# Kernel tuning notes

Hardware: AMD Instinct MI355X
Metric: run time of the kernel (lower is better)

## Reference

```python
import jax, jax.numpy as jnp
import numpy as np

B, T, STEPS = 4096, 56, 28
H, ANN, ENC, DEC = 126, 30, 20, 15
DIN = 1 + DEC + H  # decoder GRU input width = 142


def _gru_step(h, x, Wih, Whh, bih, bhh):
    # torch GRU cell math; Wih: [3H, in], Whh: [3H, H]
    gi = x @ Wih.T + bih
    gh = h @ Whh.T + bhh
    ir, iz, inn = jnp.split(gi, 3, axis=-1)
    hr, hz, hn = jnp.split(gh, 3, axis=-1)
    r = jax.nn.sigmoid(ir + hr)
    z = jax.nn.sigmoid(iz + hz)
    n = jnp.tanh(inn + r * hn)
    return (1.0 - z) * n + z * h


def setup_inputs() -> dict:
    key = jax.random.key(0)
    ks = jax.random.split(key, 23)
    p = lambda k, s: jax.random.normal(k, s, dtype=jnp.float32) * 0.08
    return {
        "ann_data": jax.random.normal(ks[0], (B, ANN), dtype=jnp.float32),
        "encoder_data": jax.random.normal(ks[1], (T, B, ENC), dtype=jnp.float32),
        "decoder_data": jax.random.normal(ks[2], (STEPS, B, DEC), dtype=jnp.float32),
        "s2h_W1": p(ks[3], (96, ANN)), "s2h_b1": p(ks[4], (96,)),
        "s2h_W2": p(ks[5], (H, 96)), "s2h_b2": p(ks[6], (H,)),
        "enc_Wih": p(ks[7], (3 * H, ENC)), "enc_Whh": p(ks[8], (3 * H, H)),
        "enc_bih": p(ks[9], (3 * H,)), "enc_bhh": p(ks[10], (3 * H,)),
        "dec_Wih": p(ks[11], (3 * H, DIN)), "dec_Whh": p(ks[12], (3 * H, H)),
        "dec_bih": p(ks[13], (3 * H,)), "dec_bhh": p(ks[14], (3 * H,)),
        "U_W": p(ks[15], (H, H)), "U_b": p(ks[16], (H,)),
        "Wl_W": p(ks[17], (H, H)), "Wl_b": p(ks[18], (H,)),
        "V_W": p(ks[19], (1, H)), "V_b": p(ks[20], (1,)),
        "h2o_W": p(ks[21], (1, H)), "h2o_b": p(ks[22], (1,)),
    }


def reference(ann_data, encoder_data, decoder_data,
              s2h_W1, s2h_b1, s2h_W2, s2h_b2,
              enc_Wih, enc_Whh, enc_bih, enc_bhh,
              dec_Wih, dec_Whh, dec_bih, dec_bhh,
              U_W, U_b, Wl_W, Wl_b, V_W, V_b, h2o_W, h2o_b):
    # static -> initial hidden: Linear(ANN,96) -> ReLU -> Linear(96,H)
    hidden = jnp.maximum(ann_data @ s2h_W1.T + s2h_b1, 0.0) @ s2h_W2.T + s2h_b2  # [B,H]

    def enc_f(h, x):
        h2 = _gru_step(h, x, enc_Wih, enc_Whh, enc_bih, enc_bhh)
        return h2, h2

    hidden, enc_out = jax.lax.scan(enc_f, hidden, encoder_data)  # enc_out: [T,B,H]

    Uo = enc_out @ U_W.T + U_b            # [T,B,H] precomputed (loop-invariant)
    gt0 = encoder_data[-1, :, 0:1]        # initial_ground, [B,1]

    def dec_f(carry, dec_x):
        h, prev = carry
        Wh = h @ Wl_W.T + Wl_b                              # [B,H]
        scores = jnp.tanh(Uo + Wh[None]) @ V_W.T + V_b      # [T,B,1]
        alpha = jax.nn.softmax(scores, axis=0)              # softmax over time
        attn = jnp.einsum('tb,tbh->bh', alpha[..., 0], enc_out)
        x = jnp.concatenate([prev, dec_x, attn], axis=1)    # [B,DIN]
        h2 = _gru_step(h, x, dec_Wih, dec_Whh, dec_bih, dec_bhh)
        out = h2 @ h2o_W.T + h2o_b                          # [B,1]
        return (h2, out), out

    _, outputs = jax.lax.scan(dec_f, (hidden, gt0), decoder_data)
    return outputs  # [STEPS, B, 1]
```

## Files before the change

### kernel.cpp

```cpp
#include <hip/hip_runtime.h>
#include <stdint.h>

typedef unsigned int u32;
typedef unsigned short u16;
typedef _Float16 f16;
typedef _Float16 f16x8 __attribute__((ext_vector_type(8)));
typedef _Float16 f16x4 __attribute__((ext_vector_type(4)));
typedef _Float16 f16x2 __attribute__((ext_vector_type(2)));
typedef float f32x4 __attribute__((ext_vector_type(4)));

constexpr int NB = 4096;
constexpr int NT = 56;
constexpr int NS = 28;
constexpr int NH = 126;
constexpr int NHP = 128;
constexpr float LOG2E = 1.4426950408889634f;

constexpr int LROW = 136;
constexpr int LB   = NT * LROW + 8;

constexpr size_t OFF_H    = 0;
constexpr size_t OFF_ENC  = 2097152;
constexpr size_t OFF_UO   = OFF_ENC + 58720256;
constexpr size_t OFF_WENC = OFF_UO + 58720256;
constexpr size_t OFF_WDEC = OFF_WENC + 122880;
constexpr size_t OFF_WL   = OFF_WDEC + 221184;
constexpr size_t OFF_UW   = OFF_WL + 32768;

__device__ __forceinline__ float fexp2(float x){ return __builtin_amdgcn_exp2f(x); }
__device__ __forceinline__ float frcp (float x){ return __builtin_amdgcn_rcpf(x); }
__device__ __forceinline__ float sigm (float x){ return frcp(1.f + fexp2(-LOG2E * x)); }
__device__ __forceinline__ float ftanh(float x){ return 1.f - 2.f * frcp(1.f + fexp2(2.f * LOG2E * x)); }
__device__ __forceinline__ float asf(u32 u){ union { u32 i; float f; } v; v.i = u; return v.f; }
__device__ __forceinline__ u16 tobf(float f){ union { float f; u32 i; } v; v.f = f;
  return (u16)((v.i + 0x7fffu + ((v.i >> 16) & 1u)) >> 16); }

__global__ void k_prep(const float* __restrict__ eWih, const float* __restrict__ eWhh,
                       const float* __restrict__ dWih, const float* __restrict__ dWhh,
                       const float* __restrict__ UW,   const float* __restrict__ Wl,
                       char* __restrict__ ws)
{
  f16* wenc = (f16*)(ws + OFF_WENC);
  f16* wdec = (f16*)(ws + OFF_WDEC);
  f16* wl   = (f16*)(ws + OFF_WL);
  f16* uw   = (f16*)(ws + OFF_UW);
  const int nE = 384 * 160, nD = 384 * 288, nW = 128 * 128;
  const int total = nE + nD + nW + nW;
  for (int i = blockIdx.x * 256 + threadIdx.x; i < total; i += gridDim.x * 256) {
    int idx = i;
    if (idx < nE) {
      const int r = idx / 160, c = idx % 160;
      float v = 0.f;
      if (r < 378) {
        if (c < 20) v = eWih[r * 20 + c];
        else if (c >= 32 && c < 158) v = eWhh[r * 126 + (c - 32)];
      }
      wenc[idx] = (f16)v; continue;
    }
    idx -= nE;
    if (idx < nD) {
      const int r = idx / 288, c = idx % 288;
      float v = 0.f;
      if (r < 378) {
        if (c < 16) v = dWih[r * 142 + c];
        else if (c >= 32 && c < 158) v = dWih[r * 142 + 16 + (c - 32)];
        else if (c >= 160 && c < 286) v = dWhh[r * 126 + (c - 160)];
      }
      wdec[idx] = (f16)v; continue;
    }
    idx -= nD;
    if (idx < nW) {
      const int r = idx >> 7, c = idx & 127;
      wl[idx] = (f16)((r < 126 && c < 126) ? Wl[r * 126 + c] : 0.f);
      continue;
    }
    idx -= nW;
    { const int r = idx >> 7, c = idx & 127;
      uw[idx] = (f16)((r < 126 && c < 126) ? UW[r * 126 + c] : 0.f); }
  }
}

__global__ __launch_bounds__(256) void k_mlp(
    const float* __restrict__ ann, const float* __restrict__ W1, const float* __restrict__ b1,
    const float* __restrict__ W2, const float* __restrict__ b2, float* __restrict__ hstate)
{
  __shared__ float anns[32][33];
  __shared__ float t1s[32][101];
  const int tid = threadIdx.x;
  const int b0 = blockIdx.x * 32;
  for (int i = tid; i < 32 * 30; i += 256)
    anns[i / 30][i % 30] = ann[(b0 + i / 30) * 30 + (i % 30)];
  __syncthreads();
  const int b = tid & 31, rg = tid >> 5;
  for (int m = rg; m < 96; m += 8) {
    float a = b1[m];
    for (int k = 0; k < 30; ++k) a += W1[m * 30 + k] * anns[b][k];
    t1s[b][m] = fmaxf(a, 0.f);
  }
  __syncthreads();
  for (int j = rg; j < NHP; j += 8) {
    float a = 0.f;
    if (j < NH) {
      a = b2[j];
      for (int k = 0; k < 96; ++k) a += W2[j * 96 + k] * t1s[b][k];
    }
    hstate[(b0 + b) * NHP + j] = a;
  }
}

__global__ __launch_bounds__(512) void k_enc(
    const float* __restrict__ xenc, const f16* __restrict__ Wenc,
    const f16* __restrict__ Uw,
    const float* __restrict__ bih, const float* __restrict__ bhh,
    const float* __restrict__ Ub,
    float* __restrict__ hstate, f16* __restrict__ encO, u16* __restrict__ uoO)
{
  __shared__ f16 av[16][296];
  const int tid = threadIdx.x;
  const int wid = tid >> 6, l = tid & 63, quad = l >> 4, col = l & 15;
  const int b0 = blockIdx.x * 16;
  const int jb = wid * 16, j = jb + col;
  const bool valid = j < NH;
  const int jc = valid ? j : NH - 1;

  const float br  = bih[jc]        + bhh[jc];
  const float bz  = bih[NH + jc]   + bhh[NH + jc];
  const float bnx = bih[2*NH + jc];
  const float bnh = bhh[2*NH + jc];
  const float ub  = Ub[jc];

  f16x8 rB[5], zB[5], nxB, nhB[4], uB[4];
  {
    const int ko = quad * 8, rr = jb + col;
#pragma unroll
    for (int kt = 0; kt < 5; ++kt) {
      rB[kt] = *(const f16x8*)&Wenc[rr * 160 + kt * 32 + ko];
      zB[kt] = *(const f16x8*)&Wenc[(NH + rr) * 160 + kt * 32 + ko];
    }
    nxB = *(const f16x8*)&Wenc[(2*NH + rr) * 160 + ko];
#pragma unroll
    for (int kt = 0; kt < 4; ++kt) {
      nhB[kt] = *(const f16x8*)&Wenc[(2*NH + rr) * 160 + 32 + kt * 32 + ko];
      uB[kt]  = *(const f16x8*)&Uw[rr * 128 + kt * 32 + ko];
    }
  }

  {
    const int bb = tid >> 5, c4 = (tid & 31) * 4;
    const float4 hv = *(const float4*)&hstate[(b0 + bb) * NHP + c4];
    av[bb][32 + c4]     = (f16)hv.x; av[bb][32 + c4 + 1] = (f16)hv.y;
    av[bb][32 + c4 + 2] = (f16)hv.z; av[bb][32 + c4 + 3] = (f16)hv.w;
  }
  if (tid < 192) { const int bb = tid / 12, p = tid % 12; av[bb][20 + p] = (f16)0.f; }
  __syncthreads();

  const int m = col, ko = quad * 8;
  for (int t = 0; t < NT; ++t) {
    const int hp = 32 + (t & 1) * 128, hq = 32 + ((t + 1) & 1) * 128;
    if (tid < 320) {
      const int bb = tid / 20, e = tid % 20;
      av[bb][e] = (f16)xenc[((size_t)t * NB + b0 + bb) * 20 + e];
    }
    __syncthreads();
    f16x8 A[5];
    A[0] = *(const f16x8*)&av[m][ko];
#pragma unroll
    for (int kt = 1; kt < 5; ++kt) A[kt] = *(const f16x8*)&av[m][hp + (kt - 1) * 32 + ko];

    f32x4 Cr = {br, br, br, br}, Cz = {bz, bz, bz, bz};
    f32x4 Cnx = {bnx, bnx, bnx, bnx}, Cnh = {bnh, bnh, bnh, bnh};
#pragma unroll
    for (int kt = 0; kt < 5; ++kt) {
      Cr = __builtin_amdgcn_mfma_f32_16x16x32_f16(A[kt], rB[kt], Cr, 0, 0, 0);
      Cz = __builtin_amdgcn_mfma_f32_16x16x32_f16(A[kt], zB[kt], Cz, 0, 0, 0);
    }
    Cnx = __builtin_amdgcn_mfma_f32_16x16x32_f16(A[0], nxB, Cnx, 0, 0, 0);
#pragma unroll
    for (int kt = 0; kt < 4; ++kt)
      Cnh = __builtin_amdgcn_mfma_f32_16x16x32_f16(A[kt + 1], nhB[kt], Cnh, 0, 0, 0);

    float hv4[4];
#pragma unroll
    for (int c = 0; c < 4; ++c) {
      const int bb = quad * 4 + c;
      const float hold = (float)av[bb][hp + j];
      const float r = sigm(Cr[c]), z = sigm(Cz[c]);
      const float n = ftanh(Cnx[c] + r * Cnh[c]);
      hv4[c] = (1.f - z) * n + z * hold;
    }
#pragma unroll
    for (int c = 0; c < 4; ++c) {
      const int bb = quad * 4 + c;
      const f16 hs = valid ? (f16)hv4[c] : (f16)0.f;
      av[bb][hq + j] = hs;
      encO[((size_t)(b0 + bb) * NT + t) * 128 + j] = hs;
    }
    if (t == NT - 1 && valid) {
#pragma unroll
      for (int c = 0; c < 4; ++c)
        hstate[(b0 + quad * 4 + c) * NHP + j] = hv4[c];
    }
    __syncthreads();

    f16x8 Ah[4];
#pragma unroll
    for (int kt = 0; kt < 4; ++kt) Ah[kt] = *(const f16x8*)&av[m][hq + kt * 32 + ko];
    f32x4 Cu = {ub, ub, ub, ub};
#pragma unroll
    for (int kt = 0; kt < 4; ++kt)
      Cu = __builtin_amdgcn_mfma_f32_16x16x32_f16(Ah[kt], uB[kt], Cu, 0, 0, 0);
#pragma unroll
    for (int c = 0; c < 4; ++c) {
      const u16 eu = tobf(fexp2(2.f * LOG2E * Cu[c]));
      uoO[((size_t)(b0 + quad * 4 + c) * NT + t) * 128 + j] = valid ? eu : (u16)0;
    }
  }
}

__global__ __launch_bounds__(512) void k_dec(
    const float* __restrict__ xdec, const float* __restrict__ xenc,
    const f16* __restrict__ Wdec, const f16* __restrict__ WlW,
    const float* __restrict__ bih, const float* __restrict__ bhh,
    const float* __restrict__ Wlb, const float* __restrict__ Vw,
    const float* __restrict__ Vb, const float* __restrict__ how,
    const float* __restrict__ hob, const float* __restrict__ hstate,
    const f16* __restrict__ encO, const u16* __restrict__ uoO,
    float* __restrict__ out)
{
  __shared__ __align__(16) u16 uoL[4 * LB];
  __shared__ __align__(16) f16 encL[4 * LB];
  __shared__ __align__(16) f16 av[5][424];
  __shared__ float EWS[4][132];
  __shared__ float scS[4][68];
  __shared__ __align__(16) f16 hows16[128];
  const int tid = threadIdx.x;
  const int wid = tid >> 6, l = tid & 63, quad = l >> 4, col = l & 15;
  const int b0 = blockIdx.x * 4;
  const int jb = wid * 16, j = jb + col;
  const bool valid = j < NH;
  const int jc = valid ? j : NH - 1;

  const float br  = bih[jc]        + bhh[jc];
  const float bz  = bih[NH + jc]   + bhh[NH + jc];
  const float bnx = bih[2*NH + jc];
  const float bnh = bhh[2*NH + jc];
  const float wb  = Wlb[jc];
  const float vb0 = Vb[0], hob0 = hob[0];

  f16x8 rB[9], zB[9], nxB[5], nhB[4], wlB[4];
  {
    const int ko = quad * 8, rr = jb + col;
#pragma unroll
    for (int kt = 0; kt < 9; ++kt) {
      rB[kt] = *(const f16x8*)&Wdec[rr * 288 + kt * 32 + ko];
      zB[kt] = *(const f16x8*)&Wdec[(NH + rr) * 288 + kt * 32 + ko];
    }
#pragma unroll
    for (int kt = 0; kt < 5; ++kt)
      nxB[kt] = *(const f16x8*)&Wdec[(2*NH + rr) * 288 + kt * 32 + ko];
#pragma unroll
    for (int kt = 0; kt < 4; ++kt) {
      nhB[kt] = *(const f16x8*)&Wdec[(2*NH + rr) * 288 + 160 + kt * 32 + ko];
      wlB[kt] = *(const f16x8*)&WlW[rr * 128 + kt * 32 + ko];
    }
  }

  const int g = tid >> 3, sub = tid & 7;
  float n2v[16], svsum = 0.f;
#pragma unroll
  for (int i = 0; i < 16; ++i) {
    const int jj = sub * 16 + i;
    const float v = (jj < NH) ? Vw[jj] : 0.f;
    n2v[i] = -2.f * v;
    svsum += v;
  }
  if (tid >= 256 && tid < 384) {
    const int q = tid - 256; hows16[q] = (f16)((q < NH) ? how[q] : 0.f);
  }
  for (int i = tid; i < 5 * 424; i += 512) av[i / 424][i % 424] = (f16)0.f;
  if (tid < 24) EWS[tid / 6][126 + tid % 6] = 0.f;
  {
    const size_t gb = (size_t)b0 * NT * 128;
    for (int i = tid; i < 4 * NT * 16; i += 512) {
      const int ch = i & 15, btr = i >> 4;
      const int bb = btr / NT, tt = btr % NT;
      const int dst = bb * LB + tt * LROW + ch * 8;
      const size_t src = gb + (size_t)btr * 128 + ch * 8;
      *(f16x8*)&uoL [dst] = *(const f16x8*)&uoO [src];
      *(f16x8*)&encL[dst] = *(const f16x8*)&encO[src];
    }
  }
  __syncthreads();
  if (tid < 128) {
    const int bb = tid >> 5, c4 = (tid & 31) * 4;
    const float4 hv = *(const float4*)&hstate[(b0 + bb) * NHP + c4];
    av[bb][160 + c4]     = (f16)hv.x; av[bb][160 + c4 + 1] = (f16)hv.y;
    av[bb][160 + c4 + 2] = (f16)hv.z; av[bb][160 + c4 + 3] = (f16)hv.w;
  }
  if (tid < 4) av[tid][0] = (f16)xenc[((size_t)(NT - 1) * NB + b0 + tid) * 20];
  __syncthreads();

  const int m = col, ko = quad * 8;
  const int arow = (m < 4) ? m : 4;
  const int pb = tid & 3, pth = (tid >> 2) & 1, pjp = tid >> 3;

  for (int s = 0; s < NS; ++s) {
    const int hp = 160 + (s & 1) * 128, hq = 160 + ((s + 1) & 1) * 128;

    {
      f16x8 Ah[4];
#pragma unroll
      for (int kt = 0; kt < 4; ++kt) Ah[kt] = *(const f16x8*)&av[arow][hp + kt * 32 + ko];
      f32x4 Cw = {wb, wb, wb, wb};
#pragma unroll
      for (int kt = 0; kt < 4; ++kt)
        Cw = __builtin_amdgcn_mfma_f32_16x16x32_f16(Ah[kt], wlB[kt], Cw, 0, 0, 0);
      if (quad == 0 && valid) {
#pragma unroll
        for (int c = 0; c < 4; ++c) EWS[c][j] = fexp2(2.f * LOG2E * Cw[c]);
      }
    }
    if (tid < 60) { const int bb = tid / 15, e = tid % 15;
      av[bb][1 + e] = (f16)xdec[((size_t)s * NB + b0 + bb) * 15 + e]; }
    __syncthreads();

    {
      const int sbb = g & 3, tb = g >> 2;
      float ew[16];
#pragma unroll
      for (int i = 0; i < 4; ++i)
        *(float4*)&ew[i * 4] = *(const float4*)&EWS[sbb][sub * 16 + i * 4];
      const u16* up0 = &uoL[sbb * LB + sub * 16];
#pragma unroll
      for (int rd = 0; rd < 4; ++rd) {
        const int t = rd * 16 + tb;
        if (t < NT) {
          const u16* up = up0 + t * LROW;
          const uint4 q0 = *(const uint4*)&up[0];
          const uint4 q1 = *(const uint4*)&up[8];
          float acc = svsum;
          const u32 wsv[8] = {q0.x, q0.y, q0.z, q0.w, q1.x, q1.y, q1.z, q1.w};
#pragma unroll
          for (int k = 0; k < 8; ++k) {
            const float p0 = fmaf(asf(wsv[k] << 16),         ew[2 * k],     1.f);
            const float p1 = fmaf(asf(wsv[k] & 0xffff0000u), ew[2 * k + 1], 1.f);
            acc = fmaf(n2v[2 * k],     frcp(p0), acc);
            acc = fmaf(n2v[2 * k + 1], frcp(p1), acc);
          }
          acc += __shfl_xor(acc, 1, 64);
          acc += __shfl_xor(acc, 2, 64);
          acc += __shfl_xor(acc, 4, 64);
          if (sub == 0) scS[sbb][t] = acc + vb0;
        }
      }
    }
    __syncthreads();

    {
      const int j0 = pjp * 2;
      const f16* er = &encL[pb * LB + j0];
      const float* scp = &scS[pb][pth * 28];
      const int tbase = pth * 28;
      float Z = 0.f, a0 = 0.f, a1 = 0.f;
#pragma unroll
      for (int i2 = 0; i2 < 28; i2 += 2) {
        const float2 scv = *(const float2*)&scp[i2];
        const float e0 = fexp2(LOG2E * scv.x);
        const float e1 = fexp2(LOG2E * scv.y);
        Z += e0 + e1;
        const f16x2 v0 = *(const f16x2*)&er[(tbase + i2    ) * LROW];
        const f16x2 v1 = *(const f16x2*)&er[(tbase + i2 + 1) * LROW];
        a0 += e0 * (float)v0[0] + e1 * (float)v1[0];
        a1 += e0 * (float)v0[1] + e1 * (float)v1[1];
      }
      a0 += __shfl_xor(a0, 4, 64);
      a1 += __shfl_xor(a1, 4, 64);
      Z  += __shfl_xor(Z, 4, 64);
      if (pth == 0) {
        const float inv = frcp(Z);
        f16x2 st; st[0] = (f16)(a0 * inv); st[1] = (f16)(a1 * inv);
        *(f16x2*)&av[pb][32 + j0] = st;
      }
    }
    __syncthreads();

    {
      f16x8 A[9];
#pragma unroll
      for (int kt = 0; kt < 5; ++kt) A[kt] = *(const f16x8*)&av[arow][kt * 32 + ko];
#pragma unroll
      for (int kt = 5; kt < 9; ++kt) A[kt] = *(const f16x8*)&av[arow][hp + (kt - 5) * 32 + ko];
      f32x4 Cr = {br, br, br, br}, Cz = {bz, bz, bz, bz};
      f32x4 Cnx = {bnx, bnx, bnx, bnx}, Cnh = {bnh, bnh, bnh, bnh};
#pragma unroll
      for (int kt = 0; kt < 9; ++kt) {
        Cr = __builtin_amdgcn_mfma_f32_16x16x32_f16(A[kt], rB[kt], Cr, 0, 0, 0);
        Cz = __builtin_amdgcn_mfma_f32_16x16x32_f16(A[kt], zB[kt], Cz, 0, 0, 0);
      }
#pragma unroll
      for (int kt = 0; kt < 5; ++kt)
        Cnx = __builtin_amdgcn_mfma_f32_16x16x32_f16(A[kt], nxB[kt], Cnx, 0, 0, 0);
#pragma unroll
      for (int kt = 0; kt < 4; ++kt)
        Cnh = __builtin_amdgcn_mfma_f32_16x16x32_f16(A[kt + 5], nhB[kt], Cnh, 0, 0, 0);
      if (quad == 0) {
#pragma unroll
        for (int c = 0; c < 4; ++c) {
          const float hold = (float)av[c][hp + j];
          const float r = sigm(Cr[c]), z = sigm(Cz[c]);
          const float n = ftanh(Cnx[c] + r * Cnh[c]);
          const float h2 = (1.f - z) * n + z * hold;
          if (valid) av[c][hq + j] = (f16)h2;
        }
      }
    }
    __syncthreads();

    if (wid == 0) {
      f16x8 Ah2[4], hB[4];
      const f16x8 zz = {};
#pragma unroll
      for (int kt = 0; kt < 4; ++kt) {
        Ah2[kt] = *(const f16x8*)&av[arow][hq + kt * 32 + ko];
        hB[kt] = (col == 0) ? *(const f16x8*)&hows16[kt * 32 + ko] : zz;
      }
      f32x4 Co = {0.f, 0.f, 0.f, 0.f};
#pragma unroll
      for (int kt = 0; kt < 4; ++kt)
        Co = __builtin_amdgcn_mfma_f32_16x16x32_f16(Ah2[kt], hB[kt], Co, 0, 0, 0);
      if (l == 0) {
#pragma unroll
        for (int c = 0; c < 4; ++c) {
          const float o = Co[c] + hob0;
          out[(size_t)s * NB + b0 + c] = o;
          av[c][0] = (f16)o;
        }
      }
    }
  }
}

extern "C" void kernel_launch(void* const* d_in, const int* in_sizes, int n_in,
                              void* d_out, int out_size, void* d_ws, size_t ws_size,
                              hipStream_t stream)
{
  const float* ann   = (const float*)d_in[0];
  const float* xenc  = (const float*)d_in[1];
  const float* xdec  = (const float*)d_in[2];
  const float* W1    = (const float*)d_in[3];
  const float* b1    = (const float*)d_in[4];
  const float* W2    = (const float*)d_in[5];
  const float* b2    = (const float*)d_in[6];
  const float* eWih  = (const float*)d_in[7];
  const float* eWhh  = (const float*)d_in[8];
  const float* ebih  = (const float*)d_in[9];
  const float* ebhh  = (const float*)d_in[10];
  const float* dWih  = (const float*)d_in[11];
  const float* dWhh  = (const float*)d_in[12];
  const float* dbih  = (const float*)d_in[13];
  const float* dbhh  = (const float*)d_in[14];
  const float* UW    = (const float*)d_in[15];
  const float* Ubias = (const float*)d_in[16];
  const float* Wl    = (const float*)d_in[17];
  const float* Wlb   = (const float*)d_in[18];
  const float* Vw    = (const float*)d_in[19];
  const float* Vb    = (const float*)d_in[20];
  const float* how   = (const float*)d_in[21];
  const float* hob   = (const float*)d_in[22];

  char* ws = (char*)d_ws;
  float* hstate = (float*)(ws + OFF_H);
  f16*   encB   = (f16*)(ws + OFF_ENC);
  u16*   uoB    = (u16*)(ws + OFF_UO);
  const f16* pWenc = (const f16*)(ws + OFF_WENC);
  const f16* pWdec = (const f16*)(ws + OFF_WDEC);
  const f16* pWl   = (const f16*)(ws + OFF_WL);
  const f16* pUW   = (const f16*)(ws + OFF_UW);

  k_prep<<<200, 256, 0, stream>>>(eWih, eWhh, dWih, dWhh, UW, Wl, ws);
  k_mlp <<<128, 256, 0, stream>>>(ann, W1, b1, W2, b2, hstate);
  k_enc <<<NB / 16, 512, 0, stream>>>(xenc, pWenc, pUW, ebih, ebhh, Ubias,
                                      hstate, encB, uoB);
  k_dec <<<NB / 4, 512, 0, stream>>>(xdec, xenc, pWdec, pWl, dbih, dbhh,
                                     Wlb, Vw, Vb, how, hob, hstate,
                                     encB, uoB, (float*)d_out);
}
```

Measured before the change: 655.3 us.

## Spread MFMA batch rows across quads, prefetch Uo rows, precompute softmax exponentials

Remaps the MFMA A-operand so batch rows land at rows 0,4,8,12 instead of 0-3. Each quad then holds one batch element in output register 0, so the GRU epilogue and the exp/output writes run on all four quads instead of only quad 0 looping four times. It also software-prefetches the next Uo row in the attention score loop and splits that loop's accumulators into four independent chains. The softmax exponential moves into the score writer, so the context pass only does FMAs with split accumulators. The catch is extra registers for the prefetch and a clamped redundant load on the last round.

```diff
diff --git a/kernel.cpp b/kernel.cpp
--- a/kernel.cpp
+++ b/kernel.cpp
@@ -301,7 +301,7 @@
   __syncthreads();
 
   const int m = col, ko = quad * 8;
-  const int arow = (m < 4) ? m : 4;
+  const int arow = ((m & 3) == 0) ? (m >> 2) : 4;
   const int pb = tid & 3, pth = (tid >> 2) & 1, pjp = tid >> 3;
 
   for (int s = 0; s < NS; ++s) {
@@ -315,10 +315,7 @@
 #pragma unroll
       for (int kt = 0; kt < 4; ++kt)
         Cw = __builtin_amdgcn_mfma_f32_16x16x32_f16(Ah[kt], wlB[kt], Cw, 0, 0, 0);
-      if (quad == 0 && valid) {
-#pragma unroll
-        for (int c = 0; c < 4; ++c) EWS[c][j] = fexp2(2.f * LOG2E * Cw[c]);
-      }
+      if (valid) EWS[quad][j] = fexp2(2.f * LOG2E * Cw[0]);
     }
     if (tid < 60) { const int bb = tid / 15, e = tid % 15;
       av[bb][1 + e] = (f16)xdec[((size_t)s * NB + b0 + bb) * 15 + e]; }
@@ -331,26 +328,35 @@
       for (int i = 0; i < 4; ++i)
         *(float4*)&ew[i * 4] = *(const float4*)&EWS[sbb][sub * 16 + i * 4];
       const u16* up0 = &uoL[sbb * LB + sub * 16];
+      uint4 q0 = *(const uint4*)&up0[tb * LROW];
+      uint4 q1 = *(const uint4*)&up0[tb * LROW + 8];
 #pragma unroll
       for (int rd = 0; rd < 4; ++rd) {
         const int t = rd * 16 + tb;
+        const u32 wsv[8] = {q0.x, q0.y, q0.z, q0.w, q1.x, q1.y, q1.z, q1.w};
+        if (rd < 3) {
+          const int tn = (t + 16 < NT) ? (t + 16) : (NT - 1);
+          q0 = *(const uint4*)&up0[tn * LROW];
+          q1 = *(const uint4*)&up0[tn * LROW + 8];
+        }
         if (t < NT) {
-          const u16* up = up0 + t * LROW;
-          const uint4 q0 = *(const uint4*)&up[0];
-          const uint4 q1 = *(const uint4*)&up[8];
-          float acc = svsum;
-          const u32 wsv[8] = {q0.x, q0.y, q0.z, q0.w, q1.x, q1.y, q1.z, q1.w};
-#pragma unroll
-          for (int k = 0; k < 8; ++k) {
-            const float p0 = fmaf(asf(wsv[k] << 16),         ew[2 * k],     1.f);
-            const float p1 = fmaf(asf(wsv[k] & 0xffff0000u), ew[2 * k + 1], 1.f);
-            acc = fmaf(n2v[2 * k],     frcp(p0), acc);
-            acc = fmaf(n2v[2 * k + 1], frcp(p1), acc);
+          float ac0 = 0.f, ac1 = 0.f, ac2 = 0.f, ac3 = 0.f;
+#pragma unroll
+          for (int k = 0; k < 8; k += 2) {
+            const float p0 = fmaf(asf(wsv[k]     << 16),          ew[2 * k],     1.f);
+            const float p1 = fmaf(asf(wsv[k]     & 0xffff0000u),  ew[2 * k + 1], 1.f);
+            const float p2 = fmaf(asf(wsv[k + 1] << 16),          ew[2 * k + 2], 1.f);
+            const float p3 = fmaf(asf(wsv[k + 1] & 0xffff0000u),  ew[2 * k + 3], 1.f);
+            ac0 = fmaf(n2v[2 * k],     frcp(p0), ac0);
+            ac1 = fmaf(n2v[2 * k + 1], frcp(p1), ac1);
+            ac2 = fmaf(n2v[2 * k + 2], frcp(p2), ac2);
+            ac3 = fmaf(n2v[2 * k + 3], frcp(p3), ac3);
           }
+          float acc = svsum + (ac0 + ac1) + (ac2 + ac3);
           acc += __shfl_xor(acc, 1, 64);
           acc += __shfl_xor(acc, 2, 64);
           acc += __shfl_xor(acc, 4, 64);
-          if (sub == 0) scS[sbb][t] = acc + vb0;
+          if (sub == 0) scS[sbb][t] = fexp2(LOG2E * (acc + vb0));
         }
       }
     }
@@ -361,18 +367,19 @@
       const f16* er = &encL[pb * LB + j0];
       const float* scp = &scS[pb][pth * 28];
       const int tbase = pth * 28;
-      float Z = 0.f, a0 = 0.f, a1 = 0.f;
+      float Z0 = 0.f, Z1 = 0.f, a00 = 0.f, a01 = 0.f, a10 = 0.f, a11 = 0.f;
 #pragma unroll
       for (int i2 = 0; i2 < 28; i2 += 2) {
-        const float2 scv = *(const float2*)&scp[i2];
-        const float e0 = fexp2(LOG2E * scv.x);
-        const float e1 = fexp2(LOG2E * scv.y);
-        Z += e0 + e1;
+        const float2 ev = *(const float2*)&scp[i2];
         const f16x2 v0 = *(const f16x2*)&er[(tbase + i2    ) * LROW];
         const f16x2 v1 = *(const f16x2*)&er[(tbase + i2 + 1) * LROW];
-        a0 += e0 * (float)v0[0] + e1 * (float)v1[0];
-        a1 += e0 * (float)v0[1] + e1 * (float)v1[1];
-      }
+        Z0 += ev.x; Z1 += ev.y;
+        a00 = fmaf(ev.x, (float)v0[0], a00);
+        a01 = fmaf(ev.y, (float)v1[0], a01);
+        a10 = fmaf(ev.x, (float)v0[1], a10);
+        a11 = fmaf(ev.y, (float)v1[1], a11);
+      }
+      float Z = Z0 + Z1, a0 = a00 + a01, a1 = a10 + a11;
       a0 += __shfl_xor(a0, 4, 64);
       a1 += __shfl_xor(a1, 4, 64);
       Z  += __shfl_xor(Z, 4, 64);
@@ -403,15 +410,12 @@
 #pragma unroll
       for (int kt = 0; kt < 4; ++kt)
         Cnh = __builtin_amdgcn_mfma_f32_16x16x32_f16(A[kt + 5], nhB[kt], Cnh, 0, 0, 0);
-      if (quad == 0) {
-#pragma unroll
-        for (int c = 0; c < 4; ++c) {
-          const float hold = (float)av[c][hp + j];
-          const float r = sigm(Cr[c]), z = sigm(Cz[c]);
-          const float n = ftanh(Cnx[c] + r * Cnh[c]);
-          const float h2 = (1.f - z) * n + z * hold;
-          if (valid) av[c][hq + j] = (f16)h2;
-        }
+      {
+        const float hold = (float)av[quad][hp + j];
+        const float r = sigm(Cr[0]), z = sigm(Cz[0]);
+        const float n = ftanh(Cnx[0] + r * Cnh[0]);
+        const float h2 = (1.f - z) * n + z * hold;
+        if (valid) av[quad][hq + j] = (f16)h2;
       }
     }
     __syncthreads();
@@ -428,13 +432,10 @@
 #pragma unroll
       for (int kt = 0; kt < 4; ++kt)
         Co = __builtin_amdgcn_mfma_f32_16x16x32_f16(Ah2[kt], hB[kt], Co, 0, 0, 0);
-      if (l == 0) {
-#pragma unroll
-        for (int c = 0; c < 4; ++c) {
-          const float o = Co[c] + hob0;
-          out[(size_t)s * NB + b0 + c] = o;
-          av[c][0] = (f16)o;
-        }
+      if (col == 0) {
+        const float o = Co[0] + hob0;
+        out[(size_t)s * NB + b0 + quad] = o;
+        av[quad][0] = (f16)o;
       }
     }
   }
```

Measured after the change: 603.4 us. 7.9% less time.
